# Kernel optimization log

Hardware: AMD Instinct MI355X
Metric: run time of the kernel (lower is better)

Reference implementation:

```python
import jax, jax.numpy as jnp
import numpy as np


def _maxpool2(x):
    # 2x2 max pool, stride 2. x: (B, C, H, W)
    B, C, H, W = x.shape
    return x.reshape(B, C, H // 2, 2, W // 2, 2).max(axis=(3, 5))


def setup_inputs() -> dict:
    key = jax.random.key(0)
    ks = jax.random.split(key, 5)
    B, C, H, W = 16, 64, 64, 64
    x = jax.random.normal(ks[0], (B, C, H, W), dtype=jnp.float32)
    Wq = jax.random.normal(ks[1], (C // 8, C), dtype=jnp.float32) * 0.05
    Wk = jax.random.normal(ks[2], (C // 8, C), dtype=jnp.float32) * 0.05
    Wv = jax.random.normal(ks[3], (C // 2, C), dtype=jnp.float32) * 0.05
    Wo = jax.random.normal(ks[4], (C, C // 2), dtype=jnp.float32) * 0.05
    gamma = jnp.float32(0.5)
    return {"x": x, "Wq": Wq, "Wk": Wk, "Wv": Wv, "Wo": Wo, "gamma": gamma}


def reference(x, Wq, Wk, Wv, Wo, gamma):
    B, C, H, W = x.shape
    # 1x1 convs (bias=False) == channel-mixing einsums
    q = jnp.einsum('oc,bchw->bohw', Wq, x)                 # (B, C/8, H, W)
    k = _maxpool2(jnp.einsum('oc,bchw->bohw', Wk, x))      # (B, C/8, H/2, W/2)
    v = _maxpool2(jnp.einsum('oc,bchw->bohw', Wv, x))      # (B, C/2, H/2, W/2)
    q = q.reshape(B, C // 8, H * W)
    k = k.reshape(B, C // 8, H * W // 4)
    v = v.reshape(B, C // 2, H * W // 4)
    # scores: (B, HW, HW/4), softmax over pooled KV axis
    w = jax.nn.softmax(jnp.einsum('bcn,bcm->bnm', q, k), axis=-1)
    o = jnp.einsum('bcm,bnm->bcn', v, w).reshape(B, C // 2, H, W)
    o = jnp.einsum('oc,bchw->bohw', Wo, o)                 # (B, C, H, W)
    return gamma * o + x
```

## Files before the change

### kernel.cpp

```cpp
#include <hip/hip_runtime.h>
#include <hip/hip_bf16.h>

typedef __attribute__((ext_vector_type(8))) short short8;
typedef __attribute__((ext_vector_type(4))) float f32x4;

#define LOG2E 1.4426950408889634f

__device__ __forceinline__ float bf2f(unsigned short s) {
    return __uint_as_float((unsigned int)s << 16);
}
__device__ __forceinline__ float fast_exp2(float x) {
#if __has_builtin(__builtin_amdgcn_exp2f)
    return __builtin_amdgcn_exp2f(x);
#else
    return __expf(x * 0.6931471805599453f);
#endif
}
__device__ __forceinline__ unsigned int cvt_pk_bf16(float lo, float hi) {
    unsigned int r;
    asm("v_cvt_pk_bf16_f32 %0, %1, %2" : "=v"(r) : "v"(lo), "v"(hi));
    return r;
}

__global__ __launch_bounds__(256, 2) void proj_pool_kernel(
    const float* __restrict__ x, const float* __restrict__ Wq,
    const float* __restrict__ Wk, const float* __restrict__ Wv,
    unsigned short* __restrict__ q_ws, unsigned short* __restrict__ k_ws,
    unsigned short* __restrict__ v_t)
{
    __shared__ __align__(16) char smem[28672];
    char* xT = smem;
    unsigned int* kv = (unsigned int*)(smem + 16384);

    const int b = blockIdx.x >> 5, s = blockIdx.x & 31;
    const int n0 = s * 128;
    const int t = threadIdx.x;
    const int w = t >> 6, lane = t & 63;
    const int l16 = lane & 15, g4 = lane >> 4;

    short8 wf[3][2];
#pragma unroll
    for (int tile = 0; tile < 3; ++tile) {
        const float* wrow;
        float scale = 1.0f;
        if (tile == 0) {
            if (l16 < 8) { wrow = Wq + l16 * 64; scale = LOG2E * 0.25f; }
            else         { wrow = Wk + (l16 - 8) * 64; }
        } else if (tile == 1) wrow = Wv + l16 * 64;
        else                  wrow = Wv + (16 + l16) * 64;
#pragma unroll
        for (int ks = 0; ks < 2; ++ks) {
            const float4 wa = *(const float4*)(wrow + ks * 32 + g4 * 8);
            const float4 wb = *(const float4*)(wrow + ks * 32 + g4 * 8 + 4);
            union { unsigned int u[4]; short8 s8; } uu;
            uu.u[0] = cvt_pk_bf16(wa.x * scale, wa.y * scale);
            uu.u[1] = cvt_pk_bf16(wa.z * scale, wa.w * scale);
            uu.u[2] = cvt_pk_bf16(wb.x * scale, wb.y * scale);
            uu.u[3] = cvt_pk_bf16(wb.z * scale, wb.w * scale);
            wf[tile][ks] = uu.s8;
        }
    }

    {
        const int nloc = (w & 1) * 64 + lane;
        const int cbase = (w >> 1) * 32;
        const float* xp = x + (size_t)b * 262144 + (size_t)cbase * 4096 + n0 + nloc;
        unsigned int pk[16];
#pragma unroll
        for (int j = 0; j < 16; ++j) {
            const float e0 = xp[(size_t)(2 * j) * 4096];
            const float e1 = xp[(size_t)(2 * j + 1) * 4096];
            pk[j] = cvt_pk_bf16(e0, e1);
        }
        char* row = xT + nloc * 128;
        const int sw = (nloc & 7) << 4;
#pragma unroll
        for (int h = 0; h < 4; ++h) {
            const uint4 u = make_uint4(pk[h*4+0], pk[h*4+1], pk[h*4+2], pk[h*4+3]);
            *(uint4*)(row + ((((cbase >> 3) + h) * 16) ^ sw)) = u;
        }
    }
    __syncthreads();

#pragma unroll
    for (int p = 0; p < 2; ++p) {
        const int tile = w * 2 + p;
        const int nl = tile * 16 + l16;
        f32x4 C0 = {0,0,0,0}, C1 = {0,0,0,0}, C2 = {0,0,0,0};
#pragma unroll
        for (int ks = 0; ks < 2; ++ks) {
            const short8 xb = *(const short8*)(xT + nl * 128 + ((((ks*4+g4)*16)) ^ ((l16&7)<<4)));
            C0 = __builtin_amdgcn_mfma_f32_16x16x32_bf16(wf[0][ks], xb, C0, 0, 0, 0);
            C1 = __builtin_amdgcn_mfma_f32_16x16x32_bf16(wf[1][ks], xb, C1, 0, 0, 0);
            C2 = __builtin_amdgcn_mfma_f32_16x16x32_bf16(wf[2][ks], xb, C2, 0, 0, 0);
        }
        const unsigned int c0lo = cvt_pk_bf16(C0[0], C0[1]);
        const unsigned int c0hi = cvt_pk_bf16(C0[2], C0[3]);
        if (g4 < 2) {
            *(uint2*)(q_ws + (size_t)(b * 4096 + n0 + nl) * 8 + g4 * 4) = make_uint2(c0lo, c0hi);
        } else {
            *(uint2*)&kv[nl * 24 + (g4 - 2) * 2] = make_uint2(c0lo, c0hi);
        }
        *(uint2*)&kv[nl * 24 + 4 + g4 * 2] =
            make_uint2(cvt_pk_bf16(C1[0], C1[1]), cvt_pk_bf16(C1[2], C1[3]));
        *(uint2*)&kv[nl * 24 + 12 + g4 * 2] =
            make_uint2(cvt_pk_bf16(C2[0], C2[1]), cvt_pk_bf16(C2[2], C2[3]));
    }
    __syncthreads();

    if (t < 128) {
        const int m = t >> 2, cg = t & 3;
        const int r0 = m * 2, r2 = m * 2 + 64;
        const int mg = s * 32 + m;
        unsigned int res[5];
#pragma unroll
        for (int i = 0; i < 5; ++i) {
            const unsigned int a  = kv[(r0    ) * 24 + cg * 5 + i];
            const unsigned int b1 = kv[(r0 + 1) * 24 + cg * 5 + i];
            const unsigned int c  = kv[(r2    ) * 24 + cg * 5 + i];
            const unsigned int d  = kv[(r2 + 1) * 24 + cg * 5 + i];
            const float lo = fmaxf(fmaxf(bf2f(a & 0xffff), bf2f(b1 & 0xffff)),
                                   fmaxf(bf2f(c & 0xffff), bf2f(d & 0xffff)));
            const float hi = fmaxf(fmaxf(bf2f(a >> 16), bf2f(b1 >> 16)),
                                   fmaxf(bf2f(c >> 16), bf2f(d >> 16)));
            res[i] = (__float_as_uint(lo) >> 16) | (__float_as_uint(hi) & 0xffff0000u);
        }
        if (cg == 0) {
            *(uint4*)(k_ws + (size_t)(b * 1024 + mg) * 8) = make_uint4(res[0], res[1], res[2], res[3]);
            v_t[((size_t)(b * 32 + 0) << 10) + mg] = (unsigned short)(res[4] & 0xffff);
            v_t[((size_t)(b * 32 + 1) << 10) + mg] = (unsigned short)(res[4] >> 16);
        } else {
            const int cvb = cg * 10 - 8;
#pragma unroll
            for (int i = 0; i < 5; ++i) {
                v_t[((size_t)(b * 32 + cvb + 2*i    ) << 10) + mg] = (unsigned short)(res[i] & 0xffff);
                v_t[((size_t)(b * 32 + cvb + 2*i + 1) << 10) + mg] = (unsigned short)(res[i] >> 16);
            }
        }
    }
}

__global__ __launch_bounds__(512, 4) void attn_out_kernel(
    const unsigned short* __restrict__ q_ws, const unsigned short* __restrict__ k_ws,
    const unsigned short* __restrict__ v_t, const float* __restrict__ Wo,
    const float* __restrict__ x, const float* __restrict__ gamma_p,
    float* __restrict__ out)
{
    __shared__ __align__(16) char smem[81920];
    short* Klds = (short*)smem;
    char*  Vb   = smem + 16384;

    const int b = blockIdx.x >> 4, n0 = (blockIdx.x & 15) * 256;
    const int t = threadIdx.x;
    const int wid = t >> 6, lane = t & 63;
    const int l16 = lane & 15, g4 = lane >> 4;

    union { uint4 u4; short8 s8; } qfA, qfB;
    qfA.u4 = *(const uint4*)(q_ws + (size_t)(b * 4096 + n0 + wid * 32 + l16) * 8);
    qfB.u4 = *(const uint4*)(q_ws + (size_t)(b * 4096 + n0 + wid * 32 + 16 + l16) * 8);

#pragma unroll
    for (int p = 0; p < 2; ++p) {
        const int mg = p * 512 + t;
        const uint4 kr = *(const uint4*)(k_ws + (size_t)(b * 1024 + mg) * 8);
        const int row = (mg & ~31) | (((mg >> 2) & 1) << 4) | (((mg >> 3) & 3) << 2) | (mg & 3);
        *(uint4*)&Klds[row * 8] = kr;
    }
    {
        const char* vsrc = (const char*)(v_t + ((size_t)b << 15));
#pragma unroll
        for (int k8 = 0; k8 < 8; ++k8) {
            const int byt = (k8 * 512 + t) * 16;
            const uint4 vv = *(const uint4*)(vsrc + byt);
            const int cv = byt >> 11, off = byt & 2047;
            *(uint4*)(Vb + cv * 2048 + (off ^ ((cv & 7) << 4))) = vv;
        }
    }

    f32x4 a0A = {0,0,0,0}, a1A = {0,0,0,0}, a0B = {0,0,0,0}, a1B = {0,0,0,0};
    float lA = 0.f, lB = 0.f;
    __syncthreads();

    const int rsw = (l16 & 7) << 4;
    for (int sl = 0; sl < 32; ++sl) {
        const int rb = sl * 32;
        const short8 A0 = *(const short8*)&Klds[(rb + l16) * 8];
        const short8 A1 = *(const short8*)&Klds[(rb + 16 + l16) * 8];
        const f32x4 z = {0,0,0,0};
        const f32x4 sA0 = __builtin_amdgcn_mfma_f32_16x16x32_bf16(A0, qfA.s8, z, 0, 0, 0);
        const f32x4 sA1 = __builtin_amdgcn_mfma_f32_16x16x32_bf16(A1, qfA.s8, z, 0, 0, 0);
        const f32x4 sB0 = __builtin_amdgcn_mfma_f32_16x16x32_bf16(A0, qfB.s8, z, 0, 0, 0);
        const f32x4 sB1 = __builtin_amdgcn_mfma_f32_16x16x32_bf16(A1, qfB.s8, z, 0, 0, 0);

        float eA[8], eB[8];
        float psA = 0.f, psB = 0.f;
#pragma unroll
        for (int i = 0; i < 4; ++i) {
            eA[i]     = fast_exp2(sA0[i]); psA += eA[i];
            eA[4 + i] = fast_exp2(sA1[i]); psA += eA[4 + i];
            eB[i]     = fast_exp2(sB0[i]); psB += eB[i];
            eB[4 + i] = fast_exp2(sB1[i]); psB += eB[4 + i];
        }
        lA += psA; lB += psB;

        union { unsigned int u[4]; short8 s8; } pbA, pbB;
        pbA.u[0] = cvt_pk_bf16(eA[0], eA[1]); pbA.u[1] = cvt_pk_bf16(eA[2], eA[3]);
        pbA.u[2] = cvt_pk_bf16(eA[4], eA[5]); pbA.u[3] = cvt_pk_bf16(eA[6], eA[7]);
        pbB.u[0] = cvt_pk_bf16(eB[0], eB[1]); pbB.u[1] = cvt_pk_bf16(eB[2], eB[3]);
        pbB.u[2] = cvt_pk_bf16(eB[4], eB[5]); pbB.u[3] = cvt_pk_bf16(eB[6], eB[7]);

        const int moff = rb * 2 + g4 * 16;
        const short8 va0 = *(const short8*)(Vb + l16 * 2048 + (moff ^ rsw));
        const short8 va1 = *(const short8*)(Vb + (l16 + 16) * 2048 + (moff ^ rsw));
        a0A = __builtin_amdgcn_mfma_f32_16x16x32_bf16(va0, pbA.s8, a0A, 0, 0, 0);
        a1A = __builtin_amdgcn_mfma_f32_16x16x32_bf16(va1, pbA.s8, a1A, 0, 0, 0);
        a0B = __builtin_amdgcn_mfma_f32_16x16x32_bf16(va0, pbB.s8, a0B, 0, 0, 0);
        a1B = __builtin_amdgcn_mfma_f32_16x16x32_bf16(va1, pbB.s8, a1B, 0, 0, 0);
    }

    {
        float l2 = lA + __shfl_xor(lA, 16); l2 += __shfl_xor(l2, 32);
        const float inv = 1.0f / l2;
        a0A *= inv; a1A *= inv;
        float l3 = lB + __shfl_xor(lB, 16); l3 += __shfl_xor(l3, 32);
        const float inv2 = 1.0f / l3;
        a0B *= inv2; a1B *= inv2;
    }

    __syncthreads();
    f32x4* o4 = (f32x4*)Vb;
    float* wo_lds = (float*)Klds;
    {
        const int nlA = wid * 32 + l16, nlB = nlA + 16;
        o4[nlA * 8 + ((g4    ) ^ (nlA & 7))] = a0A;
        o4[nlA * 8 + ((g4 + 4) ^ (nlA & 7))] = a1A;
        o4[nlB * 8 + ((g4    ) ^ (nlB & 7))] = a0B;
        o4[nlB * 8 + ((g4 + 4) ^ (nlB & 7))] = a1B;
    }
    for (int idx = t; idx < 2048; idx += 512) wo_lds[idx] = Wo[idx];
    __syncthreads();

    const float gv = gamma_p[0];
    const int n2 = t & 255;
    const int cg = t >> 8;
    float oc[32];
#pragma unroll
    for (int q8 = 0; q8 < 8; ++q8) {
        const f32x4 v = o4[n2 * 8 + (q8 ^ (n2 & 7))];
        const int cvb = (q8 >> 2) * 16 + (q8 & 3) * 4;
        oc[cvb + 0] = v[0]; oc[cvb + 1] = v[1]; oc[cvb + 2] = v[2]; oc[cvb + 3] = v[3];
    }
#pragma unroll
    for (int j = 0; j < 32; ++j) {
        const int c = cg * 32 + j;
        const f32x4* w4 = (const f32x4*)&wo_lds[c * 32];
        float a = 0.f;
#pragma unroll
        for (int q8 = 0; q8 < 8; ++q8) {
            const f32x4 wv = w4[q8];
            a += oc[q8 * 4 + 0] * wv[0] + oc[q8 * 4 + 1] * wv[1]
               + oc[q8 * 4 + 2] * wv[2] + oc[q8 * 4 + 3] * wv[3];
        }
        const size_t oidx = ((size_t)(b * 64 + c) << 12) + n0 + n2;
        out[oidx] = fmaf(gv, a, x[oidx]);
    }
}

extern "C" void kernel_launch(void* const* d_in, const int* in_sizes, int n_in,
                              void* d_out, int out_size, void* d_ws, size_t ws_size,
                              hipStream_t stream) {
    const float* x     = (const float*)d_in[0];
    const float* Wq    = (const float*)d_in[1];
    const float* Wk    = (const float*)d_in[2];
    const float* Wv    = (const float*)d_in[3];
    const float* Wo    = (const float*)d_in[4];
    const float* gamma = (const float*)d_in[5];
    float* out = (float*)d_out;

    char* ws = (char*)d_ws;
    unsigned short* q_ws = (unsigned short*)ws;
    unsigned short* k_ws = (unsigned short*)(ws + (1 << 20));
    unsigned short* v_t  = (unsigned short*)(ws + (1 << 20) + (256 << 10));

    proj_pool_kernel<<<dim3(512), dim3(256), 0, stream>>>(x, Wq, Wk, Wv, q_ws, k_ws, v_t);
    attn_out_kernel<<<dim3(256), dim3(512), 0, stream>>>(q_ws, k_ws, v_t, Wo, x, gamma, out);
}
```

Baseline: 35.37 us.

## Split attention and output projection into separate kernels with MFMA Wo projection

Splits the fused attention+Wo kernel into an attention kernel that writes bf16 outputs to a workspace, plus a separate kernel doing the Wo projection with MFMA and the residual add. The attention kernel now uses 256-thread blocks over 128 queries, which doubles the grid to 512 blocks. It stages V in two halves to cut LDS to 48KB and allow more resident blocks. This trades an extra launch and a workspace round trip, plus bf16 rounding of the attention output and Wo, for more parallelism and tensor-core use in the projection.

```diff
diff --git a/kernel.cpp b/kernel.cpp
--- a/kernel.cpp
+++ b/kernel.cpp
@@ -140,17 +140,15 @@
     }
 }
 
-__global__ __launch_bounds__(512, 4) void attn_out_kernel(
+__global__ __launch_bounds__(256, 2) void attn_kernel(
     const unsigned short* __restrict__ q_ws, const unsigned short* __restrict__ k_ws,
-    const unsigned short* __restrict__ v_t, const float* __restrict__ Wo,
-    const float* __restrict__ x, const float* __restrict__ gamma_p,
-    float* __restrict__ out)
+    const unsigned short* __restrict__ v_t, unsigned short* __restrict__ o_ws)
 {
-    __shared__ __align__(16) char smem[81920];
+    __shared__ __align__(16) char smem[49152];
     short* Klds = (short*)smem;
     char*  Vb   = smem + 16384;
 
-    const int b = blockIdx.x >> 4, n0 = (blockIdx.x & 15) * 256;
+    const int b = blockIdx.x >> 5, n0 = (blockIdx.x & 31) * 128;
     const int t = threadIdx.x;
     const int wid = t >> 6, lane = t & 63;
     const int l16 = lane & 15, g4 = lane >> 4;
@@ -160,62 +158,74 @@
     qfB.u4 = *(const uint4*)(q_ws + (size_t)(b * 4096 + n0 + wid * 32 + 16 + l16) * 8);
 
 #pragma unroll
-    for (int p = 0; p < 2; ++p) {
-        const int mg = p * 512 + t;
+    for (int p = 0; p < 4; ++p) {
+        const int mg = p * 256 + t;
         const uint4 kr = *(const uint4*)(k_ws + (size_t)(b * 1024 + mg) * 8);
         const int row = (mg & ~31) | (((mg >> 2) & 1) << 4) | (((mg >> 3) & 3) << 2) | (mg & 3);
         *(uint4*)&Klds[row * 8] = kr;
     }
-    {
-        const char* vsrc = (const char*)(v_t + ((size_t)b << 15));
-#pragma unroll
-        for (int k8 = 0; k8 < 8; ++k8) {
-            const int byt = (k8 * 512 + t) * 16;
-            const uint4 vv = *(const uint4*)(vsrc + byt);
-            const int cv = byt >> 11, off = byt & 2047;
-            *(uint4*)(Vb + cv * 2048 + (off ^ ((cv & 7) << 4))) = vv;
-        }
-    }
+    const int scv = t >> 3, sj8 = t & 7;
+    const unsigned short* vsrc0 = v_t + ((size_t)b << 15) + scv * 1024;
+    char* vdst = Vb + scv * 1024;
+    const int vsw = (scv & 7) << 4;
+    auto stageVhalf = [&](int ph) {
+#pragma unroll
+        for (int k = 0; k < 8; ++k) {
+            const int off = (k * 8 + sj8) * 16;
+            const uint4 vv = *(const uint4*)((const char*)(vsrc0 + ph * 512) + off);
+            *(uint4*)(vdst + (off ^ vsw)) = vv;
+        }
+    };
 
     f32x4 a0A = {0,0,0,0}, a1A = {0,0,0,0}, a0B = {0,0,0,0}, a1B = {0,0,0,0};
     float lA = 0.f, lB = 0.f;
+
+    stageVhalf(0);
     __syncthreads();
 
     const int rsw = (l16 & 7) << 4;
-    for (int sl = 0; sl < 32; ++sl) {
-        const int rb = sl * 32;
-        const short8 A0 = *(const short8*)&Klds[(rb + l16) * 8];
-        const short8 A1 = *(const short8*)&Klds[(rb + 16 + l16) * 8];
-        const f32x4 z = {0,0,0,0};
-        const f32x4 sA0 = __builtin_amdgcn_mfma_f32_16x16x32_bf16(A0, qfA.s8, z, 0, 0, 0);
-        const f32x4 sA1 = __builtin_amdgcn_mfma_f32_16x16x32_bf16(A1, qfA.s8, z, 0, 0, 0);
-        const f32x4 sB0 = __builtin_amdgcn_mfma_f32_16x16x32_bf16(A0, qfB.s8, z, 0, 0, 0);
-        const f32x4 sB1 = __builtin_amdgcn_mfma_f32_16x16x32_bf16(A1, qfB.s8, z, 0, 0, 0);
-
-        float eA[8], eB[8];
-        float psA = 0.f, psB = 0.f;
-#pragma unroll
-        for (int i = 0; i < 4; ++i) {
-            eA[i]     = fast_exp2(sA0[i]); psA += eA[i];
-            eA[4 + i] = fast_exp2(sA1[i]); psA += eA[4 + i];
-            eB[i]     = fast_exp2(sB0[i]); psB += eB[i];
-            eB[4 + i] = fast_exp2(sB1[i]); psB += eB[4 + i];
-        }
-        lA += psA; lB += psB;
-
-        union { unsigned int u[4]; short8 s8; } pbA, pbB;
-        pbA.u[0] = cvt_pk_bf16(eA[0], eA[1]); pbA.u[1] = cvt_pk_bf16(eA[2], eA[3]);
-        pbA.u[2] = cvt_pk_bf16(eA[4], eA[5]); pbA.u[3] = cvt_pk_bf16(eA[6], eA[7]);
-        pbB.u[0] = cvt_pk_bf16(eB[0], eB[1]); pbB.u[1] = cvt_pk_bf16(eB[2], eB[3]);
-        pbB.u[2] = cvt_pk_bf16(eB[4], eB[5]); pbB.u[3] = cvt_pk_bf16(eB[6], eB[7]);
-
-        const int moff = rb * 2 + g4 * 16;
-        const short8 va0 = *(const short8*)(Vb + l16 * 2048 + (moff ^ rsw));
-        const short8 va1 = *(const short8*)(Vb + (l16 + 16) * 2048 + (moff ^ rsw));
-        a0A = __builtin_amdgcn_mfma_f32_16x16x32_bf16(va0, pbA.s8, a0A, 0, 0, 0);
-        a1A = __builtin_amdgcn_mfma_f32_16x16x32_bf16(va1, pbA.s8, a1A, 0, 0, 0);
-        a0B = __builtin_amdgcn_mfma_f32_16x16x32_bf16(va0, pbB.s8, a0B, 0, 0, 0);
-        a1B = __builtin_amdgcn_mfma_f32_16x16x32_bf16(va1, pbB.s8, a1B, 0, 0, 0);
+#pragma unroll
+    for (int ph = 0; ph < 2; ++ph) {
+        if (ph == 1) {
+            __syncthreads();
+            stageVhalf(1);
+            __syncthreads();
+        }
+        for (int sl = 0; sl < 16; ++sl) {
+            const int rb = ph * 512 + sl * 32;
+            const short8 A0 = *(const short8*)&Klds[(rb + l16) * 8];
+            const short8 A1 = *(const short8*)&Klds[(rb + 16 + l16) * 8];
+            const f32x4 z = {0,0,0,0};
+            const f32x4 sA0 = __builtin_amdgcn_mfma_f32_16x16x32_bf16(A0, qfA.s8, z, 0, 0, 0);
+            const f32x4 sA1 = __builtin_amdgcn_mfma_f32_16x16x32_bf16(A1, qfA.s8, z, 0, 0, 0);
+            const f32x4 sB0 = __builtin_amdgcn_mfma_f32_16x16x32_bf16(A0, qfB.s8, z, 0, 0, 0);
+            const f32x4 sB1 = __builtin_amdgcn_mfma_f32_16x16x32_bf16(A1, qfB.s8, z, 0, 0, 0);
+
+            float eA[8], eB[8];
+            float psA = 0.f, psB = 0.f;
+#pragma unroll
+            for (int i = 0; i < 4; ++i) {
+                eA[i]     = fast_exp2(sA0[i]); psA += eA[i];
+                eA[4 + i] = fast_exp2(sA1[i]); psA += eA[4 + i];
+                eB[i]     = fast_exp2(sB0[i]); psB += eB[i];
+                eB[4 + i] = fast_exp2(sB1[i]); psB += eB[4 + i];
+            }
+            lA += psA; lB += psB;
+
+            union { unsigned int u[4]; short8 s8; } pbA, pbB;
+            pbA.u[0] = cvt_pk_bf16(eA[0], eA[1]); pbA.u[1] = cvt_pk_bf16(eA[2], eA[3]);
+            pbA.u[2] = cvt_pk_bf16(eA[4], eA[5]); pbA.u[3] = cvt_pk_bf16(eA[6], eA[7]);
+            pbB.u[0] = cvt_pk_bf16(eB[0], eB[1]); pbB.u[1] = cvt_pk_bf16(eB[2], eB[3]);
+            pbB.u[2] = cvt_pk_bf16(eB[4], eB[5]); pbB.u[3] = cvt_pk_bf16(eB[6], eB[7]);
+
+            const int loc = sl * 64 + g4 * 16;
+            const short8 va0 = *(const short8*)(Vb + l16 * 1024 + (loc ^ rsw));
+            const short8 va1 = *(const short8*)(Vb + (l16 + 16) * 1024 + (loc ^ rsw));
+            a0A = __builtin_amdgcn_mfma_f32_16x16x32_bf16(va0, pbA.s8, a0A, 0, 0, 0);
+            a1A = __builtin_amdgcn_mfma_f32_16x16x32_bf16(va1, pbA.s8, a1A, 0, 0, 0);
+            a0B = __builtin_amdgcn_mfma_f32_16x16x32_bf16(va0, pbB.s8, a0B, 0, 0, 0);
+            a1B = __builtin_amdgcn_mfma_f32_16x16x32_bf16(va1, pbB.s8, a1B, 0, 0, 0);
+        }
     }
 
     {
@@ -227,42 +237,66 @@
         a0B *= inv2; a1B *= inv2;
     }
 
+    {
+        const int nA = n0 + wid * 32 + l16, nB = nA + 16;
+        unsigned short* oa = o_ws + (size_t)(b * 4096 + nA) * 32;
+        unsigned short* ob = o_ws + (size_t)(b * 4096 + nB) * 32;
+        *(uint2*)(oa + g4 * 4)      = make_uint2(cvt_pk_bf16(a0A[0], a0A[1]), cvt_pk_bf16(a0A[2], a0A[3]));
+        *(uint2*)(oa + 16 + g4 * 4) = make_uint2(cvt_pk_bf16(a1A[0], a1A[1]), cvt_pk_bf16(a1A[2], a1A[3]));
+        *(uint2*)(ob + g4 * 4)      = make_uint2(cvt_pk_bf16(a0B[0], a0B[1]), cvt_pk_bf16(a0B[2], a0B[3]));
+        *(uint2*)(ob + 16 + g4 * 4) = make_uint2(cvt_pk_bf16(a1B[0], a1B[1]), cvt_pk_bf16(a1B[2], a1B[3]));
+    }
+}
+
+__global__ __launch_bounds__(256, 4) void wo_res_kernel(
+    const unsigned short* __restrict__ o_ws, const float* __restrict__ Wo,
+    const float* __restrict__ x, const float* __restrict__ gamma_p,
+    float* __restrict__ out)
+{
+    __shared__ __align__(16) short osm[64][36];
+
+    const int b = blockIdx.x >> 6, s = blockIdx.x & 63;
+    const int n0 = s * 64;
+    const int t = threadIdx.x;
+    const int wid = t >> 6, lane = t & 63;
+    const int l16 = lane & 15, g4 = lane >> 4;
+
+    {
+        const int n = t >> 2, q = t & 3;
+        const uint4 ov = *(const uint4*)(o_ws + (size_t)(b * 4096 + n0 + n) * 32 + q * 8);
+        *(uint4*)&osm[n][q * 8] = ov;
+    }
+    short8 wf[4];
+#pragma unroll
+    for (int ct = 0; ct < 4; ++ct) {
+        const float* wr = Wo + (ct * 16 + l16) * 32 + g4 * 8;
+        const float4 wa = *(const float4*)wr;
+        const float4 wb = *(const float4*)(wr + 4);
+        union { unsigned int u[4]; short8 s8; } uu;
+        uu.u[0] = cvt_pk_bf16(wa.x, wa.y); uu.u[1] = cvt_pk_bf16(wa.z, wa.w);
+        uu.u[2] = cvt_pk_bf16(wb.x, wb.y); uu.u[3] = cvt_pk_bf16(wb.z, wb.w);
+        wf[ct] = uu.s8;
+    }
+    const float gv = gamma_p[0];
     __syncthreads();
-    f32x4* o4 = (f32x4*)Vb;
-    float* wo_lds = (float*)Klds;
-    {
-        const int nlA = wid * 32 + l16, nlB = nlA + 16;
-        o4[nlA * 8 + ((g4    ) ^ (nlA & 7))] = a0A;
-        o4[nlA * 8 + ((g4 + 4) ^ (nlA & 7))] = a1A;
-        o4[nlB * 8 + ((g4    ) ^ (nlB & 7))] = a0B;
-        o4[nlB * 8 + ((g4 + 4) ^ (nlB & 7))] = a1B;
-    }
-    for (int idx = t; idx < 2048; idx += 512) wo_lds[idx] = Wo[idx];
-    __syncthreads();
-
-    const float gv = gamma_p[0];
-    const int n2 = t & 255;
-    const int cg = t >> 8;
-    float oc[32];
-#pragma unroll
-    for (int q8 = 0; q8 < 8; ++q8) {
-        const f32x4 v = o4[n2 * 8 + (q8 ^ (n2 & 7))];
-        const int cvb = (q8 >> 2) * 16 + (q8 & 3) * 4;
-        oc[cvb + 0] = v[0]; oc[cvb + 1] = v[1]; oc[cvb + 2] = v[2]; oc[cvb + 3] = v[3];
-    }
-#pragma unroll
-    for (int j = 0; j < 32; ++j) {
-        const int c = cg * 32 + j;
-        const f32x4* w4 = (const f32x4*)&wo_lds[c * 32];
-        float a = 0.f;
-#pragma unroll
-        for (int q8 = 0; q8 < 8; ++q8) {
-            const f32x4 wv = w4[q8];
-            a += oc[q8 * 4 + 0] * wv[0] + oc[q8 * 4 + 1] * wv[1]
-               + oc[q8 * 4 + 2] * wv[2] + oc[q8 * 4 + 3] * wv[3];
-        }
-        const size_t oidx = ((size_t)(b * 64 + c) << 12) + n0 + n2;
-        out[oidx] = fmaf(gv, a, x[oidx]);
+
+    const int nn = wid * 16 + l16;
+    const short8 bfr = *(const short8*)&osm[nn][g4 * 8];
+    f32x4 acc[4];
+    const f32x4 z = {0,0,0,0};
+#pragma unroll
+    for (int ct = 0; ct < 4; ++ct)
+        acc[ct] = __builtin_amdgcn_mfma_f32_16x16x32_bf16(wf[ct], bfr, z, 0, 0, 0);
+
+    const int ncol = n0 + wid * 16 + l16;
+#pragma unroll
+    for (int ct = 0; ct < 4; ++ct) {
+#pragma unroll
+        for (int i = 0; i < 4; ++i) {
+            const int c = ct * 16 + g4 * 4 + i;
+            const size_t gi = ((size_t)(b * 64 + c) << 12) + ncol;
+            out[gi] = fmaf(gv, acc[ct][i], x[gi]);
+        }
     }
 }
 
@@ -281,7 +315,9 @@
     unsigned short* q_ws = (unsigned short*)ws;
     unsigned short* k_ws = (unsigned short*)(ws + (1 << 20));
     unsigned short* v_t  = (unsigned short*)(ws + (1 << 20) + (256 << 10));
+    unsigned short* o_ws = (unsigned short*)(ws + (2 << 20) + (256 << 10));
 
     proj_pool_kernel<<<dim3(512), dim3(256), 0, stream>>>(x, Wq, Wk, Wv, q_ws, k_ws, v_t);
-    attn_out_kernel<<<dim3(256), dim3(512), 0, stream>>>(q_ws, k_ws, v_t, Wo, x, gamma, out);
-}
+    attn_kernel<<<dim3(512), dim3(256), 0, stream>>>(q_ws, k_ws, v_t, o_ws);
+    wo_res_kernel<<<dim3(1024), dim3(256), 0, stream>>>(o_ws, Wo, x, gamma, out);
+}
```

After: 33.80 us (median of 3 runs). 4.4% less time.
